# Optimization experiments

Measured on AMD Instinct MI355X. Metric: run time of the kernel, lower is better.

The kernel has to match this reference:

```python
import jax, jax.numpy as jnp
import numpy as np

LN_EPS = 1e-5

def _ln(x, g, b):
    m = x.mean(-1, keepdims=True)
    v = jnp.mean((x - m) ** 2, axis=-1, keepdims=True)
    return (x - m) * jax.lax.rsqrt(v + LN_EPS) * g + b


def setup_inputs() -> dict:
    key = jax.random.key(0)
    ks = jax.random.split(key, 8)
    B, S, H = 8, 4096, 2048
    V, L, E = 32, 8, 64   # vocab_size, symbol seq_len, embedding_dim
    sc = 0.02
    d = {}
    d["hidden_states"] = jax.random.normal(ks[0], (B, S, H), jnp.float32)
    # uniform in (0,1) for Gumbel noise: g = -log(-log(u))
    d["gumbel_u"] = jax.random.uniform(ks[1], (B, L, V), jnp.float32, 1e-6, 1.0 - 1e-6)
    d["enc_w1"] = jax.random.normal(ks[2], (256, H), jnp.float32) * sc
    d["enc_b1"] = jnp.zeros((256,), jnp.float32)
    d["ln1_g"] = jnp.ones((256,), jnp.float32)
    d["ln1_b"] = jnp.zeros((256,), jnp.float32)
    d["enc_w2"] = jax.random.normal(ks[3], (L * V, 256), jnp.float32) * sc
    d["enc_b2"] = jnp.zeros((L * V,), jnp.float32)
    d["embed"] = jax.random.normal(ks[4], (V, E), jnp.float32) * sc
    d["dec_w1"] = jax.random.normal(ks[5], (256, L * E), jnp.float32) * sc
    d["dec_b1"] = jnp.zeros((256,), jnp.float32)
    d["ln2_g"] = jnp.ones((256,), jnp.float32)
    d["ln2_b"] = jnp.zeros((256,), jnp.float32)
    d["dec_w2"] = jax.random.normal(ks[6], (H, 256), jnp.float32) * sc
    d["dec_b2"] = jnp.zeros((H,), jnp.float32)
    return d


def reference(hidden_states, gumbel_u, enc_w1, enc_b1, ln1_g, ln1_b, enc_w2, enc_b2,
              embed, dec_w1, dec_b1, ln2_g, ln2_b, dec_w2, dec_b2):
    V, L, TAU = 32, 8, 1.0
    B, S, H = hidden_states.shape
    E = embed.shape[1]
    # encode: mean-pool over sequence, then MLP -> logits [B, L, V]
    pooled = hidden_states.mean(axis=1)
    h = _ln(pooled @ enc_w1.T + enc_b1, ln1_g, ln1_b)
    h = jax.nn.gelu(h, approximate=False)
    logits = (h @ enc_w2.T + enc_b2).reshape(B, L, V)
    # gumbel-softmax with straight-through (hard) estimator
    g = -jnp.log(-jnp.log(gumbel_u))
    y_soft = jax.nn.softmax((logits + g) / TAU, axis=-1)
    idx = jnp.argmax(y_soft, axis=-1)
    y_hard = jax.nn.one_hot(idx, V, dtype=y_soft.dtype)
    soft_symbols = y_hard - jax.lax.stop_gradient(y_soft) + y_soft
    # decode: embed symbols, flatten, MLP back to hidden size
    emb = jnp.einsum('blv,ve->ble', soft_symbols, embed).reshape(B, L * E)
    dh = _ln(emb @ dec_w1.T + dec_b1, ln2_g, ln2_b)
    dh = jax.nn.gelu(dh, approximate=False)
    decoded = dh @ dec_w2.T + dec_b2            # [B, H]
    # residual + 0.1 * broadcast over sequence
    return hidden_states + 0.1 * decoded[:, None, :]
```

## Files before the change

### kernel.cpp

```cpp
#include <hip/hip_runtime.h>
#include <math.h>

#define B 8
#define S 4096
#define H 2048
#define VOC 32
#define LSYM 8
#define EMB 64

__global__ __launch_bounds__(256) void pool_partial(const float* __restrict__ hid,
                                                    float* __restrict__ part,
                                                    int chunk) {
    const int hb = blockIdx.x;
    const int b  = blockIdx.y;
    const int sp = blockIdx.z;
    const int t  = threadIdx.x;
    const int h4 = hb * 1024 + t * 4;
    float4 acc = {0.f, 0.f, 0.f, 0.f};
    const float* base = hid + (size_t)b * S * H + h4;
    const int s0 = sp * chunk;
    for (int s = 0; s < chunk; ++s) {
        const float4 v = *reinterpret_cast<const float4*>(base + (size_t)(s0 + s) * H);
        acc.x += v.x; acc.y += v.y; acc.z += v.z; acc.w += v.w;
    }
    *reinterpret_cast<float4*>(part + ((size_t)sp * B + b) * H + h4) = acc;
}

__global__ __launch_bounds__(256) void pool_reduce(const float* __restrict__ part,
                                                   float* __restrict__ pooled,
                                                   int split) {
    const int i4 = blockIdx.x * 256 + threadIdx.x;
    if (i4 >= B * H / 4) return;
    float4 acc = {0.f, 0.f, 0.f, 0.f};
    for (int sp = 0; sp < split; ++sp) {
        const float4 v = *reinterpret_cast<const float4*>(part + (size_t)sp * B * H + (size_t)i4 * 4);
        acc.x += v.x; acc.y += v.y; acc.z += v.z; acc.w += v.w;
    }
    const float inv = 1.0f / (float)S;
    acc.x *= inv; acc.y *= inv; acc.z *= inv; acc.w *= inv;
    *reinterpret_cast<float4*>(pooled + (size_t)i4 * 4) = acc;
}

__global__ __launch_bounds__(256) void enc1_matvec(const float* __restrict__ pooled,
                                                   const float* __restrict__ ew1,
                                                   const float* __restrict__ eb1,
                                                   float* __restrict__ out1) {
    const int wv   = (blockIdx.x * 256 + threadIdx.x) >> 6;
    const int lane = threadIdx.x & 63;
    const int b = wv >> 8, t = wv & 255;
    const float4* wrow = reinterpret_cast<const float4*>(ew1 + (size_t)t * H);
    const float4* prow = reinterpret_cast<const float4*>(pooled + b * H);
    float acc = 0.f;
#pragma unroll
    for (int i = 0; i < 8; ++i) {
        const float4 w = wrow[lane + 64 * i];
        const float4 p = prow[lane + 64 * i];
        acc += w.x * p.x + w.y * p.y + w.z * p.z + w.w * p.w;
    }
    for (int off = 32; off; off >>= 1) acc += __shfl_xor(acc, off, 64);
    if (lane == 0) out1[b * 256 + t] = acc + eb1[t];
}

__device__ __forceinline__ float block_sum256(float x, float* red) {
    const int t = threadIdx.x;
    red[t] = x;
    __syncthreads();
    for (int s = 128; s > 0; s >>= 1) {
        if (t < s) red[t] += red[t + s];
        __syncthreads();
    }
    const float r = red[0];
    __syncthreads();
    return r;
}

__global__ __launch_bounds__(256) void mlp_middle(
    const float* __restrict__ out1, const float* __restrict__ gu,
    const float* __restrict__ g1,  const float* __restrict__ bb1,
    const float* __restrict__ ew2, const float* __restrict__ eb2,
    const float* __restrict__ emb_tab,
    const float* __restrict__ dw1, const float* __restrict__ db1,
    const float* __restrict__ g2,  const float* __restrict__ bb2,
    float* __restrict__ hs2) {
    __shared__ float red[256];
    __shared__ float hs[256];
    __shared__ float es[LSYM * EMB];

    const int b = blockIdx.x;
    const int t = threadIdx.x;

    float acc = out1[b * 256 + t];
    {
        const float m = block_sum256(acc, red) * (1.0f / 256.0f);
        const float d = acc - m;
        const float v = block_sum256(d * d, red) * (1.0f / 256.0f);
        float x = d * rsqrtf(v + 1e-5f) * g1[t] + bb1[t];
        x = 0.5f * x * (1.0f + erff(x * 0.70710678118654752f));
        hs[t] = x;
    }
    __syncthreads();

    float z;
    {
        float a2 = eb2[t];
        const float* w2row = ew2 + t * 256;
        for (int k = 0; k < 256; k += 4) {
            const float4 w = *reinterpret_cast<const float4*>(w2row + k);
            a2 += w.x * hs[k] + w.y * hs[k + 1] + w.z * hs[k + 2] + w.w * hs[k + 3];
        }
        const float u = gu[b * 256 + t];
        z = a2 - logf(-logf(u));
    }

    {
        int   bi = t & 31;
        float bz = z;
        for (int off = 16; off; off >>= 1) {
            const float oz = __shfl_xor(bz, off, 32);
            const int   oi = __shfl_xor(bi, off, 32);
            if (oz > bz || (oz == bz && oi < bi)) { bz = oz; bi = oi; }
        }
        const int l = t >> 5, v32 = t & 31;
        es[l * EMB + v32]      = emb_tab[bi * EMB + v32];
        es[l * EMB + 32 + v32] = emb_tab[bi * EMB + 32 + v32];
    }
    __syncthreads();

    float a3 = db1[t];
    {
        const float* d1row = dw1 + t * (LSYM * EMB);
        for (int k = 0; k < LSYM * EMB; k += 4) {
            const float4 w = *reinterpret_cast<const float4*>(d1row + k);
            a3 += w.x * es[k] + w.y * es[k + 1] + w.z * es[k + 2] + w.w * es[k + 3];
        }
    }
    {
        const float m2 = block_sum256(a3, red) * (1.0f / 256.0f);
        const float dd = a3 - m2;
        const float vv = block_sum256(dd * dd, red) * (1.0f / 256.0f);
        float y = dd * rsqrtf(vv + 1e-5f) * g2[t] + bb2[t];
        y = 0.5f * y * (1.0f + erff(y * 0.70710678118654752f));
        hs2[b * 256 + t] = y;
    }
}

__global__ __launch_bounds__(256) void dec2_matvec(const float* __restrict__ hs2,
                                                   const float* __restrict__ dw2,
                                                   const float* __restrict__ db2,
                                                   float* __restrict__ dec_sc) {
    const int wv   = (blockIdx.x * 256 + threadIdx.x) >> 6;
    const int lane = threadIdx.x & 63;
    const int b = wv >> 11, j = wv & 2047;
    const float4 w = reinterpret_cast<const float4*>(dw2 + (size_t)j * 256)[lane];
    const float4 h = reinterpret_cast<const float4*>(hs2 + b * 256)[lane];
    float acc = w.x * h.x + w.y * h.y + w.z * h.z + w.w * h.w;
    for (int off = 32; off; off >>= 1) acc += __shfl_xor(acc, off, 64);
    if (lane == 0) dec_sc[b * 2048 + j] = 0.1f * (acc + db2[j]);
}

__global__ __launch_bounds__(256) void residual_add(const float* __restrict__ hid,
                                                    const float* __restrict__ dec,
                                                    float* __restrict__ out,
                                                    size_t n4) {
    size_t i = (size_t)blockIdx.x * blockDim.x + threadIdx.x;
    const size_t stride = (size_t)gridDim.x * blockDim.x;
    const float4* __restrict__ hv4 = reinterpret_cast<const float4*>(hid);
    const float4* __restrict__ dv4 = reinterpret_cast<const float4*>(dec);
    float4* __restrict__ ov4 = reinterpret_cast<float4*>(out);
    for (; i < n4; i += stride) {
        const float4 hv = hv4[i];
        const size_t b  = i >> 21;
        const size_t h4 = i & (H / 4 - 1);
        const float4 dv = dv4[b * (H / 4) + h4];
        float4 o;
        o.x = hv.x + dv.x; o.y = hv.y + dv.y; o.z = hv.z + dv.z; o.w = hv.w + dv.w;
        ov4[i] = o;
    }
}

extern "C" void kernel_launch(void* const* d_in, const int* in_sizes, int n_in,
                              void* d_out, int out_size, void* d_ws, size_t ws_size,
                              hipStream_t stream) {
    const float* hid   = (const float*)d_in[0];
    const float* gu    = (const float*)d_in[1];
    const float* ew1   = (const float*)d_in[2];
    const float* eb1   = (const float*)d_in[3];
    const float* g1    = (const float*)d_in[4];
    const float* bb1   = (const float*)d_in[5];
    const float* ew2   = (const float*)d_in[6];
    const float* eb2   = (const float*)d_in[7];
    const float* emb   = (const float*)d_in[8];
    const float* dw1   = (const float*)d_in[9];
    const float* db1   = (const float*)d_in[10];
    const float* g2    = (const float*)d_in[11];
    const float* bb2   = (const float*)d_in[12];
    const float* dw2   = (const float*)d_in[13];
    const float* db2   = (const float*)d_in[14];
    float* out = (float*)d_out;

    const size_t avail_floats = ws_size / 4;
    int split = 64;
    while (split > 1 && (size_t)(split + 3) * B * H > avail_floats) split >>= 1;
    const int chunk = S / split;

    float* part   = (float*)d_ws;
    float* pooled = part + (size_t)split * B * H;
    float* dec_sc = pooled + (size_t)B * H;
    float* out1   = dec_sc + (size_t)B * H;
    float* hs2    = out1 + (size_t)B * 256;

    pool_partial<<<dim3(H / 1024, B, split), 256, 0, stream>>>(hid, part, chunk);
    pool_reduce<<<(B * H / 4 + 255) / 256, 256, 0, stream>>>(part, pooled, split);
    enc1_matvec<<<B * 256 / 4, 256, 0, stream>>>(pooled, ew1, eb1, out1);
    mlp_middle<<<B, 256, 0, stream>>>(out1, gu, g1, bb1, ew2, eb2, emb,
                                      dw1, db1, g2, bb2, hs2);
    dec2_matvec<<<B * 2048 / 4, 256, 0, stream>>>(hs2, dw2, db2, dec_sc);
    const size_t n4 = (size_t)B * S * H / 4;
    residual_add<<<2048, 256, 0, stream>>>(hid, dec_sc, out, n4);
}
```

Baseline: 215.6 us.

## Stream contiguous slabs in pooling and use nontemporal stores in residual add

Each pool_partial block now reads a contiguous slab of rows covering the full hidden width, using two independent accumulators, instead of a strided 1024-column slice. The sequence split doubles to 128, so the grid keeps a similar block count. The residual_add output is written with nontemporal stores so the 512MB output does not pollute the cache. The cost is a larger partial buffer that pool_reduce must read back.

```diff
diff --git a/kernel.cpp b/kernel.cpp
--- a/kernel.cpp
+++ b/kernel.cpp
@@ -8,22 +8,27 @@
 #define LSYM 8
 #define EMB 64
 
+typedef float f32x4 __attribute__((ext_vector_type(4)));
+
 __global__ __launch_bounds__(256) void pool_partial(const float* __restrict__ hid,
                                                     float* __restrict__ part,
                                                     int chunk) {
-    const int hb = blockIdx.x;
+    const int sp = blockIdx.x;
     const int b  = blockIdx.y;
-    const int sp = blockIdx.z;
     const int t  = threadIdx.x;
-    const int h4 = hb * 1024 + t * 4;
-    float4 acc = {0.f, 0.f, 0.f, 0.f};
-    const float* base = hid + (size_t)b * S * H + h4;
-    const int s0 = sp * chunk;
-    for (int s = 0; s < chunk; ++s) {
-        const float4 v = *reinterpret_cast<const float4*>(base + (size_t)(s0 + s) * H);
-        acc.x += v.x; acc.y += v.y; acc.z += v.z; acc.w += v.w;
-    }
-    *reinterpret_cast<float4*>(part + ((size_t)sp * B + b) * H + h4) = acc;
+    const float* slab = hid + (size_t)b * S * H + (size_t)sp * chunk * H;
+    const int iters = chunk * (H / 1024);
+    float4 a0 = {0.f, 0.f, 0.f, 0.f};
+    float4 a1 = {0.f, 0.f, 0.f, 0.f};
+    for (int i = 0; i < iters; i += 2) {
+        const float4 v0 = *reinterpret_cast<const float4*>(slab + (size_t)i * 1024 + t * 4);
+        const float4 v1 = *reinterpret_cast<const float4*>(slab + (size_t)(i + 1) * 1024 + t * 4);
+        a0.x += v0.x; a0.y += v0.y; a0.z += v0.z; a0.w += v0.w;
+        a1.x += v1.x; a1.y += v1.y; a1.z += v1.z; a1.w += v1.w;
+    }
+    float* dst = part + ((size_t)sp * B + b) * H;
+    *reinterpret_cast<float4*>(dst + t * 4)        = a0;
+    *reinterpret_cast<float4*>(dst + 1024 + t * 4) = a1;
 }
 
 __global__ __launch_bounds__(256) void pool_reduce(const float* __restrict__ part,
@@ -166,15 +171,15 @@
     const size_t stride = (size_t)gridDim.x * blockDim.x;
     const float4* __restrict__ hv4 = reinterpret_cast<const float4*>(hid);
     const float4* __restrict__ dv4 = reinterpret_cast<const float4*>(dec);
-    float4* __restrict__ ov4 = reinterpret_cast<float4*>(out);
+    f32x4* __restrict__ ov4 = reinterpret_cast<f32x4*>(out);
     for (; i < n4; i += stride) {
         const float4 hv = hv4[i];
         const size_t b  = i >> 21;
         const size_t h4 = i & (H / 4 - 1);
         const float4 dv = dv4[b * (H / 4) + h4];
-        float4 o;
+        f32x4 o;
         o.x = hv.x + dv.x; o.y = hv.y + dv.y; o.z = hv.z + dv.z; o.w = hv.w + dv.w;
-        ov4[i] = o;
+        __builtin_nontemporal_store(o, &ov4[i]);
     }
 }
 
@@ -199,7 +204,7 @@
     float* out = (float*)d_out;
 
     const size_t avail_floats = ws_size / 4;
-    int split = 64;
+    int split = 128;
     while (split > 1 && (size_t)(split + 3) * B * H > avail_floats) split >>= 1;
     const int chunk = S / split;
 
@@ -209,7 +214,7 @@
     float* out1   = dec_sc + (size_t)B * H;
     float* hs2    = out1 + (size_t)B * 256;
 
-    pool_partial<<<dim3(H / 1024, B, split), 256, 0, stream>>>(hid, part, chunk);
+    pool_partial<<<dim3(split, B), 256, 0, stream>>>(hid, part, chunk);
     pool_reduce<<<(B * H / 4 + 255) / 256, 256, 0, stream>>>(part, pooled, split);
     enc1_matvec<<<B * 256 / 4, 256, 0, stream>>>(pooled, ew1, eb1, out1);
     mlp_middle<<<B, 256, 0, stream>>>(out1, gu, g1, bb1, ew2, eb2, emb,
```

Result: no change. 219.3 us (+1.7%).
